# Kernel tuning notes

Measured on AMD Instinct MI355X. Metric: run time of the kernel, lower is better.

## Reference

```python
import jax, jax.numpy as jnp
import numpy as np

KH, KW = 3, 3
STRIDE, PAD, DIL = 1, 1, 1
DG = 1  # deformable groups


def setup_inputs() -> dict:
    key = jax.random.key(0)
    k1, k2, k3, k4 = jax.random.split(key, 4)
    B, C, H, W, O = 4, 64, 128, 128, 64
    x = jax.random.normal(k1, (B, C, H, W), jnp.float32)
    weight = jax.random.normal(k2, (O, C, KH, KW), jnp.float32) * 0.05
    bias = jnp.zeros((O,), jnp.float32)
    # offset/mask conv params (zero-init in original; small random here so
    # the bilinear sampling path is actually exercised)
    om_weight = jax.random.normal(k3, (DG * 3 * KH * KW, C, KH, KW), jnp.float32) * 0.01
    om_bias = jax.random.normal(k4, (DG * 3 * KH * KW,), jnp.float32) * 0.01
    return {"x": x, "weight": weight, "bias": bias,
            "om_weight": om_weight, "om_bias": om_bias}


def _dcn(x, weight, bias, om_weight, om_bias):
    B, C, H, W = x.shape
    O = weight.shape[0]
    K = KH * KW
    Cg = C // DG

    # --- offset/mask conv (plain conv2d) ---
    om = jax.lax.conv_general_dilated(
        x, om_weight, (STRIDE, STRIDE), [(PAD, PAD), (PAD, PAD)],
        dimension_numbers=("NCHW", "OIHW", "NCHW"))
    om = om + om_bias[None, :, None, None]
    Ho, Wo = om.shape[2], om.shape[3]
    o1, o2, m = jnp.split(om, 3, axis=1)            # each (B, DG*K, Ho, Wo)
    off_y = o1.reshape(B, DG, K, Ho, Wo)
    off_x = o2.reshape(B, DG, K, Ho, Wo)
    mask = jax.nn.sigmoid(m).reshape(B, DG, K, Ho, Wo)

    # --- fractional sampling positions per kernel tap ---
    ky = jnp.repeat(jnp.arange(KH), KW).astype(jnp.float32)   # (K,)
    kx = jnp.tile(jnp.arange(KW), KH).astype(jnp.float32)
    base_y = (jnp.arange(Ho, dtype=jnp.float32) * STRIDE - PAD)
    base_x = (jnp.arange(Wo, dtype=jnp.float32) * STRIDE - PAD)
    py = off_y + base_y[None, None, None, :, None] + (ky * DIL)[None, None, :, None, None]
    px = off_x + base_x[None, None, None, None, :] + (kx * DIL)[None, None, :, None, None]

    y0 = jnp.floor(py)
    x0 = jnp.floor(px)
    ly = py - y0
    lx = px - x0
    y0i = y0.astype(jnp.int32)
    x0i = x0.astype(jnp.int32)

    xg = x.reshape(B, DG, Cg, H * W)
    # gather spatial samples per (batch, group), broadcast over channels
    gather = jax.vmap(jax.vmap(lambda feat, idx: jnp.take(feat, idx, axis=-1)))

    def corner(yc, xc, w):
        valid = (yc >= 0) & (yc < H) & (xc >= 0) & (xc < W)
        idx = jnp.clip(yc, 0, H - 1) * W + jnp.clip(xc, 0, W - 1)  # (B,DG,K,Ho,Wo)
        v = gather(xg, idx.reshape(B, DG, -1)).reshape(B, DG, Cg, K, Ho, Wo)
        w = jnp.where(valid, w, 0.0)
        return v * w[:, :, None]  # zero-padded bilinear corner

    val = (corner(y0i,     x0i,     (1 - ly) * (1 - lx))
         + corner(y0i,     x0i + 1, (1 - ly) * lx)
         + corner(y0i + 1, x0i,     ly * (1 - lx))
         + corner(y0i + 1, x0i + 1, ly * lx))
    val = val * mask[:, :, None]                    # (B,DG,Cg,K,Ho,Wo)

    w4 = weight.reshape(O, DG, Cg, K)
    out = jnp.einsum("ogck,bgckhw->bohw", w4, val) + bias[None, :, None, None]
    return out


def reference(x, weight, bias, om_weight, om_bias):
    return _dcn(x, weight, bias, om_weight, om_bias)
```

## Files before the change

### kernel.cpp

```cpp
#include <hip/hip_runtime.h>
#include <hip/hip_fp16.h>
#include <math.h>

#define BB 4
#define CC 64
#define HH 128
#define WW 128
#define OO 64
#define HWW (HH * WW)

typedef _Float16 f16x8 __attribute__((ext_vector_type(8)));
typedef float f32x4 __attribute__((ext_vector_type(4)));

#define WHF_OFF  0
#define WOMH_OFF 73728

__device__ inline __half2 u2h(unsigned u) {
    union { unsigned u; __half2 h; } c; c.u = u; return c.h;
}
__device__ inline unsigned h2u(__half2 h) {
    union { __half2 h; unsigned u; } c; c.h = h; return c.u;
}

__global__ void prep_kernel(const float* __restrict__ weight,
                            const float* __restrict__ om_weight,
                            unsigned short* __restrict__ whf,
                            unsigned short* __restrict__ womh)
{
    int d = blockIdx.x * 256 + threadIdx.x;
    if (d < 18 * 4 * 64 * 8) {
        int j  = d & 7;
        int l  = (d >> 3) & 63;
        int og = (d >> 9) & 3;
        int ch = d >> 11;
        int o  = og * 16 + (l & 15);
        int kk = (l >> 4) * 8 + j;
        int c  = (ch / 9) * 32 + kk;
        int tap = ch % 9;
        float w = weight[(o * CC + c) * 9 + tap];
        whf[d] = __half_as_ushort(__float2half_rn(w));
    }
    int d2 = d - 18 * 4 * 64 * 8;
    if (d2 >= 0 && d2 < 18 * 2 * 64 * 8) {
        int j  = d2 & 7;
        int l  = (d2 >> 3) & 63;
        int og = (d2 >> 9) & 1;
        int ch = d2 >> 10;
        int o  = og * 16 + (l & 15);
        int kk = (l >> 4) * 8 + j;
        int c  = (ch / 9) * 32 + kk;
        int tap = ch % 9;
        float w = (o < 27) ? om_weight[(o * CC + c) * 9 + tap] : 0.f;
        womh[d2] = __half_as_ushort(__float2half_rn(w));
    }
}

__global__ void __launch_bounds__(256, 4)
fused_kernel(const float* __restrict__ x,
             const unsigned short* __restrict__ whf,
             const unsigned short* __restrict__ womh,
             const float* __restrict__ bias,
             const float* __restrict__ om_bias,
             float* __restrict__ out)
{
    __shared__ __align__(16) uint4 Xw[8 * 180];
    __shared__ __align__(16) uint4 vex[2][32][9];
    __shared__ __align__(16) uint4 swth4[288];
    __shared__ int sidx[288];

    int t    = threadIdx.x;
    int lane = t & 63;
    int wv   = t >> 6;

    int bid = blockIdx.x;
    int b   = bid >> 9;
    int r   = bid & 511;
    int ho  = r >> 2;
    int w0  = (r & 3) << 5;

    {
        const float* xb = x + (size_t)b * CC * HWW;
#pragma unroll 1
        for (int i = t; i < 8 * 180; i += 256) {
            int cg  = i / 180;
            int pos = i - cg * 180;
            int rr  = pos / 36;
            int cc2 = pos - rr * 36;
            int gy = ho - 2 + rr, gx = w0 - 2 + cc2;
            bool ok = (gy >= 0) & (gy < HH) & (gx >= 0) & (gx < WW);
            int gi = ok ? gy * WW + gx : 0;
            const float* xc = xb + (size_t)cg * 8 * HWW + gi;
            float v0 = xc[0],       v1 = xc[HWW],     v2 = xc[2 * HWW], v3 = xc[3 * HWW];
            float v4 = xc[4 * HWW], v5 = xc[5 * HWW], v6 = xc[6 * HWW], v7 = xc[7 * HWW];
            if (!ok) { v0=0.f; v1=0.f; v2=0.f; v3=0.f; v4=0.f; v5=0.f; v6=0.f; v7=0.f; }
            uint4 p;
            p.x = h2u(__floats2half2_rn(v0, v1));
            p.y = h2u(__floats2half2_rn(v2, v3));
            p.z = h2u(__floats2half2_rn(v4, v5));
            p.w = h2u(__floats2half2_rn(v6, v7));
            Xw[cg * 180 + pos] = p;
        }
    }
    __syncthreads();

    f32x4 accom = (f32x4){0.f, 0.f, 0.f, 0.f};
    {
        int og = wv & 1;
        int s  = wv >> 1;
        int pix_s = s * 16 + (lane & 15);
        int oct   = lane >> 4;
#pragma unroll 1
        for (int ch = 0; ch < 18; ch++) {
            int half = ch / 9;
            int tap  = ch - half * 9;
            int ky = tap / 3, kx = tap - ky * 3;
            int pos = (ky + 1) * 36 + pix_s + kx + 1;
            union { f16x8 v; uint4 u; } B;
            B.u = Xw[(half * 4 + oct) * 180 + pos];
            const f16x8 a0 = *(const f16x8*)&womh[((size_t)(ch * 2 + og) * 64 + lane) * 8];
            accom = __builtin_amdgcn_mfma_f32_16x16x32_f16(a0, B.v, accom, 0, 0, 0);
        }
    }

    float* omL = (float*)&vex[0][0][0];
    {
        int og = wv & 1, s = wv >> 1;
#pragma unroll
        for (int rg = 0; rg < 4; rg++) {
            int m = og * 16 + (lane >> 4) * 4 + rg;
            if (m < 27) {
                int pp = s * 16 + (lane & 15);
                float v = accom[rg] + om_bias[m];
                if (m >= 18) v = 1.f / (1.f + expf(-v));
                omL[m * 32 + pp] = v;
            }
        }
    }
    __syncthreads();

#pragma unroll 1
    for (int it = t; it < 288; it += 256) {
        int k  = it >> 5;
        int pp = it & 31;
        float oy = omL[k * 32 + pp];
        float ox = omL[(9 + k) * 32 + pp];
        float mm = omL[(18 + k) * 32 + pp];
        int ky = k / 3, kx = k - ky * 3;
        float py = oy + (float)(ho + ky - 1);
        float px = ox + (float)(w0 + pp + kx - 1);
        float fy = floorf(py), fx = floorf(px);
        float ly = py - fy, lx = px - fx;
        int y0 = (int)fy, x0 = (int)fx;
        bool vy0 = (y0 >= 0) & (y0 < HH);
        bool vy1 = (y0 + 1 >= 0) & (y0 + 1 < HH);
        bool vx0 = (x0 >= 0) & (x0 < WW);
        bool vx1 = (x0 + 1 >= 0) & (x0 + 1 < WW);
        float w00 = (vy0 & vx0) ? (1.f - ly) * (1.f - lx) * mm : 0.f;
        float w01 = (vy0 & vx1) ? (1.f - ly) * lx * mm : 0.f;
        float w10 = (vy1 & vx0) ? ly * (1.f - lx) * mm : 0.f;
        float w11 = (vy1 & vx1) ? ly * lx * mm : 0.f;
        uint4 wp;
        wp.x = h2u(__float2half2_rn(w00));
        wp.y = h2u(__float2half2_rn(w01));
        wp.z = h2u(__float2half2_rn(w10));
        wp.w = h2u(__float2half2_rn(w11));
        swth4[it] = wp;
        bool inw = (y0 >= ho - 2) & (y0 <= ho + 1) & (x0 >= w0 - 2) & (x0 <= w0 + 32);
        int y0c = min(max(y0, -8), 135);
        int x0c = min(max(x0, -8), 135);
        sidx[it] = ((y0c + 16) << 16) | ((x0c + 16) & 0xFFFF)
                 | (inw ? 0 : (int)0x80000000);
    }
    __syncthreads();

    int og2  = wv >> 1;
    int s2   = wv & 1;
    int pixl = lane & 15;
    int oct  = lane >> 4;

    f32x4 acc[2];
    acc[0] = (f32x4){0.f, 0.f, 0.f, 0.f};
    acc[1] = (f32x4){0.f, 0.f, 0.f, 0.f};

    {
        int pix = t & 31;
        int cg  = t >> 5;
#pragma unroll 1
        for (int tap = 0; tap < 9; tap++) {
            int buf  = tap & 1;
            int item = tap * 32 + pix;
            uint4 wp = swth4[item];
            int sv = sidx[item];
            int y0 = ((sv >> 16) & 0x7FFF) - 16;
            int x0 = (sv & 0xFFFF) - 16;
            const f16x8 a00 = *(const f16x8*)&whf[((size_t)(tap * 4 + og2 * 2 + 0) * 64 + lane) * 8];
            const f16x8 a01 = *(const f16x8*)&whf[((size_t)(tap * 4 + og2 * 2 + 1) * 64 + lane) * 8];
            const f16x8 a10 = *(const f16x8*)&whf[((size_t)((9 + tap) * 4 + og2 * 2 + 0) * 64 + lane) * 8];
            const f16x8 a11 = *(const f16x8*)&whf[((size_t)((9 + tap) * 4 + og2 * 2 + 1) * 64 + lane) * 8];

            uint4 payload;
            if (sv >= 0) {
                int o00 = (y0 - ho + 2) * 36 + (x0 - w0 + 2);
                const uint4* Xrow = &Xw[cg * 180];
                uint4 c00 = Xrow[o00];
                uint4 c01 = Xrow[o00 + 1];
                uint4 c10 = Xrow[o00 + 36];
                uint4 c11 = Xrow[o00 + 37];
                __half2 w00 = u2h(wp.x), w01 = u2h(wp.y);
                __half2 w10 = u2h(wp.z), w11 = u2h(wp.w);
                __half2 vA = __hmul2(w00, u2h(c00.x));
                vA = __hfma2(w01, u2h(c01.x), vA);
                vA = __hfma2(w10, u2h(c10.x), vA);
                vA = __hfma2(w11, u2h(c11.x), vA);
                __half2 vB = __hmul2(w00, u2h(c00.y));
                vB = __hfma2(w01, u2h(c01.y), vB);
                vB = __hfma2(w10, u2h(c10.y), vB);
                vB = __hfma2(w11, u2h(c11.y), vB);
                __half2 vC = __hmul2(w00, u2h(c00.z));
                vC = __hfma2(w01, u2h(c01.z), vC);
                vC = __hfma2(w10, u2h(c10.z), vC);
                vC = __hfma2(w11, u2h(c11.z), vC);
                __half2 vD = __hmul2(w00, u2h(c00.w));
                vD = __hfma2(w01, u2h(c01.w), vD);
                vD = __hfma2(w10, u2h(c10.w), vD);
                vD = __hfma2(w11, u2h(c11.w), vD);
                payload.x = h2u(vA); payload.y = h2u(vB);
                payload.z = h2u(vC); payload.w = h2u(vD);
            } else {
                const float* xg = x + ((size_t)(b * CC + cg * 8)) * HWW;
                float w00f = __low2float(u2h(wp.x)), w01f = __low2float(u2h(wp.y));
                float w10f = __low2float(u2h(wp.z)), w11f = __low2float(u2h(wp.w));
                int cy0 = min(max(y0, 0), HH - 1), cy1 = min(max(y0 + 1, 0), HH - 1);
                int cx0 = min(max(x0, 0), WW - 1), cx1 = min(max(x0 + 1, 0), WW - 1);
                int i00 = cy0 * WW + cx0, i01 = cy0 * WW + cx1;
                int i10 = cy1 * WW + cx0, i11 = cy1 * WW + cx1;
                float vv[8];
#pragma unroll
                for (int j = 0; j < 8; j++) {
                    const float* xc = xg + (size_t)j * HWW;
                    vv[j] = w00f * xc[i00] + w01f * xc[i01]
                          + w10f * xc[i10] + w11f * xc[i11];
                }
                payload.x = h2u(__floats2half2_rn(vv[0], vv[1]));
                payload.y = h2u(__floats2half2_rn(vv[2], vv[3]));
                payload.z = h2u(__floats2half2_rn(vv[4], vv[5]));
                payload.w = h2u(__floats2half2_rn(vv[6], vv[7]));
            }
            vex[buf][pix][cg] = payload;
            __syncthreads();
            {
                union { f16x8 v; uint4 u; } B0, B1;
                B0.u = vex[buf][s2 * 16 + pixl][oct];
                B1.u = vex[buf][s2 * 16 + pixl][4 + oct];
                acc[0] = __builtin_amdgcn_mfma_f32_16x16x32_f16(a00, B0.v, acc[0], 0, 0, 0);
                acc[1] = __builtin_amdgcn_mfma_f32_16x16x32_f16(a01, B0.v, acc[1], 0, 0, 0);
                acc[0] = __builtin_amdgcn_mfma_f32_16x16x32_f16(a10, B1.v, acc[0], 0, 0, 0);
                acc[1] = __builtin_amdgcn_mfma_f32_16x16x32_f16(a11, B1.v, acc[1], 0, 0, 0);
            }
        }
    }

    int prow = ho * WW + w0;
#pragma unroll
    for (int a = 0; a < 2; a++) {
#pragma unroll
        for (int rg = 0; rg < 4; rg++) {
            int o  = (og2 * 2 + a) * 16 + (lane >> 4) * 4 + rg;
            int pp = s2 * 16 + pixl;
            out[((size_t)(b * OO + o)) * HWW + prow + pp] = acc[a][rg] + bias[o];
        }
    }
}

extern "C" void kernel_launch(void* const* d_in, const int* in_sizes, int n_in,
                              void* d_out, int out_size, void* d_ws, size_t ws_size,
                              hipStream_t stream)
{
    (void)in_sizes; (void)n_in; (void)out_size; (void)ws_size;
    const float* x      = (const float*)d_in[0];
    const float* weight = (const float*)d_in[1];
    const float* bias   = (const float*)d_in[2];
    const float* om_w   = (const float*)d_in[3];
    const float* om_b   = (const float*)d_in[4];
    float* out = (float*)d_out;
    char*  ws  = (char*)d_ws;

    unsigned short* whf  = (unsigned short*)(ws + WHF_OFF);
    unsigned short* womh = (unsigned short*)(ws + WOMH_OFF);

    int prep_n = 18 * 4 * 64 * 8 + 18 * 2 * 64 * 8;
    prep_kernel<<<(prep_n + 255) / 256, 256, 0, stream>>>(weight, om_w, whf, womh);

    int nblk = BB * HH * (WW / 32);
    fused_kernel<<<nblk, 256, 0, stream>>>(x, whf, womh, bias, om_b, out);
}
```

Baseline: 109.7 us.

## Feed bilinear samples directly into MFMA registers, split-K across waves with LDS reduction

The main loop now has each wave compute the bilinear samples for its own channel half and pass them straight into the MFMA B operand, with no LDS staging buffer. The old loop wrote samples to LDS and called __syncthreads once per tap. Each wave now covers all 64 output channels (four accumulators) for half of the input channels. The two halves are summed through an LDS reduction buffer before the store. This removes nine block barriers and the LDS round trip, at the cost of more accumulator registers, twice the weight fragment loads per wave, and a final reduction step.

```diff
diff --git a/kernel.cpp b/kernel.cpp
--- a/kernel.cpp
+++ b/kernel.cpp
@@ -64,9 +64,9 @@
              float* __restrict__ out)
 {
     __shared__ __align__(16) uint4 Xw[8 * 180];
-    __shared__ __align__(16) uint4 vex[2][32][9];
     __shared__ __align__(16) uint4 swth4[288];
     __shared__ int sidx[288];
+    __shared__ __align__(16) f32x4 red[2 * 4 * 64];
 
     int t    = threadIdx.x;
     int lane = t & 63;
@@ -122,7 +122,7 @@
         }
     }
 
-    float* omL = (float*)&vex[0][0][0];
+    float* omL = (float*)&red[0];
     {
         int og = wv & 1, s = wv >> 1;
 #pragma unroll
@@ -173,101 +173,105 @@
     }
     __syncthreads();
 
-    int og2  = wv >> 1;
-    int s2   = wv & 1;
-    int pixl = lane & 15;
-    int oct  = lane >> 4;
-
-    f32x4 acc[2];
+    int kc    = wv & 1;
+    int s2    = wv >> 1;
+    int pixl  = lane & 15;
+    int oct   = lane >> 4;
+    int cg    = kc * 4 + oct;
+    int pix32 = s2 * 16 + pixl;
+
+    f32x4 acc[4];
     acc[0] = (f32x4){0.f, 0.f, 0.f, 0.f};
     acc[1] = (f32x4){0.f, 0.f, 0.f, 0.f};
-
-    {
-        int pix = t & 31;
-        int cg  = t >> 5;
+    acc[2] = (f32x4){0.f, 0.f, 0.f, 0.f};
+    acc[3] = (f32x4){0.f, 0.f, 0.f, 0.f};
+
+    const uint4* Xplane = &Xw[cg * 180];
+    const unsigned short* wb = whf + ((size_t)(kc * 36) * 64 + lane) * 8;
+
 #pragma unroll 1
-        for (int tap = 0; tap < 9; tap++) {
-            int buf  = tap & 1;
-            int item = tap * 32 + pix;
-            uint4 wp = swth4[item];
-            int sv = sidx[item];
-            int y0 = ((sv >> 16) & 0x7FFF) - 16;
-            int x0 = (sv & 0xFFFF) - 16;
-            const f16x8 a00 = *(const f16x8*)&whf[((size_t)(tap * 4 + og2 * 2 + 0) * 64 + lane) * 8];
-            const f16x8 a01 = *(const f16x8*)&whf[((size_t)(tap * 4 + og2 * 2 + 1) * 64 + lane) * 8];
-            const f16x8 a10 = *(const f16x8*)&whf[((size_t)((9 + tap) * 4 + og2 * 2 + 0) * 64 + lane) * 8];
-            const f16x8 a11 = *(const f16x8*)&whf[((size_t)((9 + tap) * 4 + og2 * 2 + 1) * 64 + lane) * 8];
-
-            uint4 payload;
-            if (sv >= 0) {
-                int o00 = (y0 - ho + 2) * 36 + (x0 - w0 + 2);
-                const uint4* Xrow = &Xw[cg * 180];
-                uint4 c00 = Xrow[o00];
-                uint4 c01 = Xrow[o00 + 1];
-                uint4 c10 = Xrow[o00 + 36];
-                uint4 c11 = Xrow[o00 + 37];
-                __half2 w00 = u2h(wp.x), w01 = u2h(wp.y);
-                __half2 w10 = u2h(wp.z), w11 = u2h(wp.w);
-                __half2 vA = __hmul2(w00, u2h(c00.x));
-                vA = __hfma2(w01, u2h(c01.x), vA);
-                vA = __hfma2(w10, u2h(c10.x), vA);
-                vA = __hfma2(w11, u2h(c11.x), vA);
-                __half2 vB = __hmul2(w00, u2h(c00.y));
-                vB = __hfma2(w01, u2h(c01.y), vB);
-                vB = __hfma2(w10, u2h(c10.y), vB);
-                vB = __hfma2(w11, u2h(c11.y), vB);
-                __half2 vC = __hmul2(w00, u2h(c00.z));
-                vC = __hfma2(w01, u2h(c01.z), vC);
-                vC = __hfma2(w10, u2h(c10.z), vC);
-                vC = __hfma2(w11, u2h(c11.z), vC);
-                __half2 vD = __hmul2(w00, u2h(c00.w));
-                vD = __hfma2(w01, u2h(c01.w), vD);
-                vD = __hfma2(w10, u2h(c10.w), vD);
-                vD = __hfma2(w11, u2h(c11.w), vD);
-                payload.x = h2u(vA); payload.y = h2u(vB);
-                payload.z = h2u(vC); payload.w = h2u(vD);
-            } else {
-                const float* xg = x + ((size_t)(b * CC + cg * 8)) * HWW;
-                float w00f = __low2float(u2h(wp.x)), w01f = __low2float(u2h(wp.y));
-                float w10f = __low2float(u2h(wp.z)), w11f = __low2float(u2h(wp.w));
-                int cy0 = min(max(y0, 0), HH - 1), cy1 = min(max(y0 + 1, 0), HH - 1);
-                int cx0 = min(max(x0, 0), WW - 1), cx1 = min(max(x0 + 1, 0), WW - 1);
-                int i00 = cy0 * WW + cx0, i01 = cy0 * WW + cx1;
-                int i10 = cy1 * WW + cx0, i11 = cy1 * WW + cx1;
-                float vv[8];
-#pragma unroll
-                for (int j = 0; j < 8; j++) {
-                    const float* xc = xg + (size_t)j * HWW;
-                    vv[j] = w00f * xc[i00] + w01f * xc[i01]
-                          + w10f * xc[i10] + w11f * xc[i11];
-                }
-                payload.x = h2u(__floats2half2_rn(vv[0], vv[1]));
-                payload.y = h2u(__floats2half2_rn(vv[2], vv[3]));
-                payload.z = h2u(__floats2half2_rn(vv[4], vv[5]));
-                payload.w = h2u(__floats2half2_rn(vv[6], vv[7]));
+    for (int tap = 0; tap < 9; tap++) {
+        int item = tap * 32 + pix32;
+        uint4 wp = swth4[item];
+        int sv = sidx[item];
+        int y0 = ((sv >> 16) & 0x7FFF) - 16;
+        int x0 = (sv & 0xFFFF) - 16;
+        const f16x8 a0 = *(const f16x8*)&wb[(size_t)(tap * 4 + 0) * 512];
+        const f16x8 a1 = *(const f16x8*)&wb[(size_t)(tap * 4 + 1) * 512];
+        const f16x8 a2 = *(const f16x8*)&wb[(size_t)(tap * 4 + 2) * 512];
+        const f16x8 a3 = *(const f16x8*)&wb[(size_t)(tap * 4 + 3) * 512];
+
+        uint4 payload;
+        if (sv >= 0) {
+            int o00 = (y0 - ho + 2) * 36 + (x0 - w0 + 2);
+            uint4 c00 = Xplane[o00];
+            uint4 c01 = Xplane[o00 + 1];
+            uint4 c10 = Xplane[o00 + 36];
+            uint4 c11 = Xplane[o00 + 37];
+            __half2 w00 = u2h(wp.x), w01 = u2h(wp.y);
+            __half2 w10 = u2h(wp.z), w11 = u2h(wp.w);
+            __half2 vA = __hmul2(w00, u2h(c00.x));
+            vA = __hfma2(w01, u2h(c01.x), vA);
+            vA = __hfma2(w10, u2h(c10.x), vA);
+            vA = __hfma2(w11, u2h(c11.x), vA);
+            __half2 vB = __hmul2(w00, u2h(c00.y));
+            vB = __hfma2(w01, u2h(c01.y), vB);
+            vB = __hfma2(w10, u2h(c10.y), vB);
+            vB = __hfma2(w11, u2h(c11.y), vB);
+            __half2 vC = __hmul2(w00, u2h(c00.z));
+            vC = __hfma2(w01, u2h(c01.z), vC);
+            vC = __hfma2(w10, u2h(c10.z), vC);
+            vC = __hfma2(w11, u2h(c11.z), vC);
+            __half2 vD = __hmul2(w00, u2h(c00.w));
+            vD = __hfma2(w01, u2h(c01.w), vD);
+            vD = __hfma2(w10, u2h(c10.w), vD);
+            vD = __hfma2(w11, u2h(c11.w), vD);
+            payload.x = h2u(vA); payload.y = h2u(vB);
+            payload.z = h2u(vC); payload.w = h2u(vD);
+        } else {
+            const float* xg = x + ((size_t)(b * CC + cg * 8)) * HWW;
+            float w00f = __low2float(u2h(wp.x)), w01f = __low2float(u2h(wp.y));
+            float w10f = __low2float(u2h(wp.z)), w11f = __low2float(u2h(wp.w));
+            int cy0 = min(max(y0, 0), HH - 1), cy1 = min(max(y0 + 1, 0), HH - 1);
+            int cx0 = min(max(x0, 0), WW - 1), cx1 = min(max(x0 + 1, 0), WW - 1);
+            int i00 = cy0 * WW + cx0, i01 = cy0 * WW + cx1;
+            int i10 = cy1 * WW + cx0, i11 = cy1 * WW + cx1;
+            float vv[8];
+#pragma unroll
+            for (int j = 0; j < 8; j++) {
+                const float* xc = xg + (size_t)j * HWW;
+                vv[j] = w00f * xc[i00] + w01f * xc[i01]
+                      + w10f * xc[i10] + w11f * xc[i11];
             }
-            vex[buf][pix][cg] = payload;
-            __syncthreads();
-            {
-                union { f16x8 v; uint4 u; } B0, B1;
-                B0.u = vex[buf][s2 * 16 + pixl][oct];
-                B1.u = vex[buf][s2 * 16 + pixl][4 + oct];
-                acc[0] = __builtin_amdgcn_mfma_f32_16x16x32_f16(a00, B0.v, acc[0], 0, 0, 0);
-                acc[1] = __builtin_amdgcn_mfma_f32_16x16x32_f16(a01, B0.v, acc[1], 0, 0, 0);
-                acc[0] = __builtin_amdgcn_mfma_f32_16x16x32_f16(a10, B1.v, acc[0], 0, 0, 0);
-                acc[1] = __builtin_amdgcn_mfma_f32_16x16x32_f16(a11, B1.v, acc[1], 0, 0, 0);
+            payload.x = h2u(__floats2half2_rn(vv[0], vv[1]));
+            payload.y = h2u(__floats2half2_rn(vv[2], vv[3]));
+            payload.z = h2u(__floats2half2_rn(vv[4], vv[5]));
+            payload.w = h2u(__floats2half2_rn(vv[6], vv[7]));
+        }
+        union { f16x8 v; uint4 u; } Bf;
+        Bf.u = payload;
+        acc[0] = __builtin_amdgcn_mfma_f32_16x16x32_f16(a0, Bf.v, acc[0], 0, 0, 0);
+        acc[1] = __builtin_amdgcn_mfma_f32_16x16x32_f16(a1, Bf.v, acc[1], 0, 0, 0);
+        acc[2] = __builtin_amdgcn_mfma_f32_16x16x32_f16(a2, Bf.v, acc[2], 0, 0, 0);
+        acc[3] = __builtin_amdgcn_mfma_f32_16x16x32_f16(a3, Bf.v, acc[3], 0, 0, 0);
+    }
+
+    if (kc == 1) {
+#pragma unroll
+        for (int og = 0; og < 4; og++)
+            red[(s2 * 4 + og) * 64 + lane] = acc[og];
+    }
+    __syncthreads();
+    if (kc == 0) {
+        int prow = ho * WW + w0;
+#pragma unroll
+        for (int og = 0; og < 4; og++) {
+            f32x4 v = acc[og] + red[(s2 * 4 + og) * 64 + lane];
+#pragma unroll
+            for (int rg = 0; rg < 4; rg++) {
+                int o = og * 16 + (lane >> 4) * 4 + rg;
+                out[((size_t)(b * OO + o)) * HWW + prow + pix32] = v[rg] + bias[o];
             }
-        }
-    }
-
-    int prow = ho * WW + w0;
-#pragma unroll
-    for (int a = 0; a < 2; a++) {
-#pragma unroll
-        for (int rg = 0; rg < 4; rg++) {
-            int o  = (og2 * 2 + a) * 16 + (lane >> 4) * 4 + rg;
-            int pp = s2 * 16 + pixl;
-            out[((size_t)(b * OO + o)) * HWW + prow + pp] = acc[a][rg] + bias[o];
         }
     }
 }
```

New measurement: 109.6 us. No clear change (-0.0%).
